# Performance work log

Hardware: AMD Instinct MI355X
Metric: run time of the kernel (lower is better)

The kernel has to match this reference:

```python
import jax, jax.numpy as jnp
import numpy as np

EMBEDDING_DIM = 512
MODEL_DIM = EMBEDDING_DIM
B, S = 32, 2048


def setup_inputs() -> dict:
    key = jax.random.key(0)
    ks = jax.random.split(key, 9)
    d, m = EMBEDDING_DIM, MODEL_DIM
    # xavier_uniform bounds
    def xavier(k, shape):
        fan_out, fan_in = shape
        lim = jnp.sqrt(6.0 / (fan_in + fan_out))
        return jax.random.uniform(k, shape, jnp.float32, -lim, lim)
    return {
        "query": jax.random.normal(ks[0], (B, d), jnp.float32),
        "keys": jax.random.normal(ks[1], (B, S, 2 * d), jnp.float32),
        "key_padding_mask": jax.random.randint(ks[2], (B, S), 0, 2) > 0,
        "Wa_w": xavier(ks[3], (m, d)),
        "Wa_b": jnp.zeros((m,), jnp.float32),
        "Ua_w": xavier(ks[4], (m, 2 * d)),
        "Ua_b": jnp.zeros((m,), jnp.float32),
        "Va_w": xavier(ks[5], (1, m)),
        "Va_b": jnp.zeros((1,), jnp.float32),
    }


def reference(query, keys, key_padding_mask, Wa_w, Wa_b, Ua_w, Ua_b, Va_w, Va_b):
    # Wa(query): [B, M]; Ua(keys): [B, S, M]
    wq = query @ Wa_w.T + Wa_b                      # [B, M]
    uk = jnp.einsum('bse,me->bsm', keys, Ua_w) + Ua_b  # [B, S, M]
    e = jnp.tanh(wq[:, None, :] + uk)               # [B, S, M]
    scores = jnp.einsum('bsm,om->bos', e, Va_w) + Va_b[None, :, None]  # [B, 1, S]
    scores = jnp.where(key_padding_mask[:, None, :], -jnp.inf, scores)
    attn = jax.nn.softmax(scores, axis=-1)          # [B, 1, S]
    context = jnp.einsum('bos,bse->boe', attn, keys)  # [B, 1, 2*EMBEDDING_DIM]
    return context
```

## Files before the change

### kernel.cpp

```cpp
#include <hip/hip_runtime.h>
#include <hip/hip_bf16.h>
#include <cstdint>
#include <cstddef>

#define B_   32
#define S_   2048
#define D_   512
#define K2D  1024
#define M_   512

#define WS_WQ     0
#define WS_FLAG   16384
#define WS_DENOM  16448
#define WS_UAB16  16512

typedef __attribute__((ext_vector_type(8))) short bf16x8;
typedef __attribute__((ext_vector_type(4))) float f32x4;

__device__ __forceinline__ float tanh_fast(float x) {
    float e = __expf(2.0f * x);
    return 1.0f - 2.0f * __builtin_amdgcn_rcpf(e + 1.0f);
}

union Pack8 { bf16x8 v; __hip_bfloat162 h[4]; };
__device__ __forceinline__ bf16x8 cvt8(float4 a, float4 b) {
    Pack8 p;
    p.h[0] = __float22bfloat162_rn(make_float2(a.x, a.y));
    p.h[1] = __float22bfloat162_rn(make_float2(a.z, a.w));
    p.h[2] = __float22bfloat162_rn(make_float2(b.x, b.y));
    p.h[3] = __float22bfloat162_rn(make_float2(b.z, b.w));
    return p.v;
}

__device__ __forceinline__ void gl_lds16(const void* g, void* l) {
    __builtin_amdgcn_global_load_lds(
        (const __attribute__((address_space(1))) unsigned int*)g,
        (__attribute__((address_space(3))) unsigned int*)l, 16, 0, 0);
}

__global__ __launch_bounds__(256) void k_prep(const float* __restrict__ query,
                                              const float* __restrict__ Wa_w,
                                              const float* __restrict__ Wa_b,
                                              const unsigned int* __restrict__ maskw,
                                              const float* __restrict__ Ua_w,
                                              float* __restrict__ wq,
                                              float* __restrict__ out,
                                              int* __restrict__ flag,
                                              float* __restrict__ denom,
                                              ushort* __restrict__ Ub16) {
    const int blk = blockIdx.x, t = threadIdx.x;
    if (blk < 256) {
        const int tid = blk * 256 + t;
        if (tid < 32768) out[tid] = 0.f;
        if (tid < 32) denom[tid] = 0.f;
        const int o = tid >> 2, sub = tid & 3;
        const int bq = o >> 9, m = o & 511;
        const float4* q = (const float4*)(query + (size_t)bq * D_ + sub * 128);
        const float4* w = (const float4*)(Wa_w + (size_t)m * D_ + sub * 128);
        float acc = 0.f;
#pragma unroll 8
        for (int i = 0; i < 32; ++i) {
            float4 qv = q[i], wv = w[i];
            acc = fmaf(qv.x, wv.x, acc);
            acc = fmaf(qv.y, wv.y, acc);
            acc = fmaf(qv.z, wv.z, acc);
            acc = fmaf(qv.w, wv.w, acc);
        }
        acc += __shfl_down(acc, 2, 64);
        acc += __shfl_down(acc, 1, 64);
        if (sub == 0) wq[o] = acc + Wa_b[m];
    } else if (blk == 256) {
        __shared__ int found;
        if (t == 0) found = 0;
        __syncthreads();
        int f = 0;
#pragma unroll
        for (int i = 0; i < 8; ++i)
            if (maskw[i * 256 + t] > 1u) f = 1;
        if (f) atomicOr(&found, 1);
        __syncthreads();
        if (t == 0) *flag = found;
    } else {
        const int i = ((blk - 257) * 256 + t) * 8;
        float4 a = *(const float4*)(Ua_w + i);
        float4 b = *(const float4*)(Ua_w + i + 4);
        *(bf16x8*)(Ub16 + i) = cvt8(a, b);
    }
}

__global__ __launch_bounds__(512, 2) void k_main(const float* __restrict__ keys,
                                                 const ushort* __restrict__ Ub16,
                                                 const float* __restrict__ Ua_b,
                                                 const float* __restrict__ Va_w,
                                                 const float* __restrict__ wq,
                                                 const void* __restrict__ mask,
                                                 const int* __restrict__ flag,
                                                 float* __restrict__ denom,
                                                 float* __restrict__ out) {
    __shared__ __align__(16) unsigned char smem[163840];
    unsigned char* Abase = smem;
    unsigned char* Bbase = smem + 32768;

    const int grp = blockIdx.x;
    const int b   = grp >> 4;
    const int s0  = (grp & 15) * 128;

    const int t = threadIdx.x;
    const int wave = t >> 6, lane = t & 63;
    const int q = lane >> 4, r = lane & 15;
    const int sw = (wave >> 2) * 64;
    const int mw = (wave & 3) * 128;

    const int arow = t >> 2, ac = (t & 3) * 2;
    const float* Ag = keys + ((size_t)(b * S_ + s0 + arow)) * K2D + ac * 8;
    const int ad0 = arow * 128 + ((ac ^ (arow & 7)) * 16);
    const int ad1 = arow * 128 + (((ac + 1) ^ (arow & 7)) * 16);

    const int brl = lane >> 3, bcl = lane & 7;
    const ushort* Bg = Ub16 + (size_t)(64 * wave + brl) * K2D + (bcl ^ brl) * 8;

    f32x4 acc[4][8];
#pragma unroll
    for (int i = 0; i < 4; ++i)
#pragma unroll
        for (int j = 0; j < 8; ++j) acc[i][j] = (f32x4){0.f, 0.f, 0.f, 0.f};

    {
        const float4* g = (const float4*)Ag;
        float4 f0 = g[0], f1 = g[1], f2 = g[2], f3 = g[3];
#pragma unroll
        for (int p = 0; p < 8; ++p)
            gl_lds16(Bg + (size_t)(8 * p) * K2D,
                     Bbase + (64 * wave + 8 * p) * 128);
        *(bf16x8*)(Abase + ad0) = cvt8(f0, f1);
        *(bf16x8*)(Abase + ad1) = cvt8(f2, f3);
        __syncthreads();
    }

    for (int kt = 0; kt < 16; ++kt) {
        const int cur = kt & 1, nxt = cur ^ 1;
        unsigned char* Acur = Abase + cur * 16384;
        unsigned char* Bcur = Bbase + cur * 65536;

        float4 f0, f1, f2, f3;
        if (kt < 15) {
            const int ko = (kt + 1) * 64;
            const float4* g = (const float4*)(Ag + ko);
            f0 = g[0]; f1 = g[1]; f2 = g[2]; f3 = g[3];
#pragma unroll
            for (int p = 0; p < 8; ++p)
                gl_lds16(Bg + (size_t)(8 * p) * K2D + ko,
                         Bbase + nxt * 65536 + (64 * wave + 8 * p) * 128);
        }

#pragma unroll
        for (int ks = 0; ks < 2; ++ks) {
            bf16x8 af[4], bf[8];
            const int lc = ks * 4 + q;
            const int pco = ((lc ^ (r & 7)) * 16);
#pragma unroll
            for (int i = 0; i < 4; ++i)
                af[i] = *(const bf16x8*)(Acur + (sw + i * 16 + r) * 128 + pco);
#pragma unroll
            for (int j = 0; j < 8; ++j)
                bf[j] = *(const bf16x8*)(Bcur + (mw + j * 16 + r) * 128 + pco);
#pragma unroll
            for (int i = 0; i < 4; ++i)
#pragma unroll
                for (int j = 0; j < 8; ++j)
                    acc[i][j] = __builtin_amdgcn_mfma_f32_16x16x32_bf16(
                        af[i], bf[j], acc[i][j], 0, 0, 0);
        }

        if (kt < 15) {
            unsigned char* An = Abase + nxt * 16384;
            *(bf16x8*)(An + ad0) = cvt8(f0, f1);
            *(bf16x8*)(An + ad1) = cvt8(f2, f3);
        }
        __syncthreads();
    }

    float vaw[8], wqb[8];
#pragma unroll
    for (int j = 0; j < 8; ++j) {
        int m = mw + 16 * j + r;
        vaw[j] = Va_w[m];
        wqb[j] = wq[b * M_ + m] + Ua_b[m];
    }
    float* red = (float*)smem;
    const int col = (wave & 3) * 16 + r;
#pragma unroll
    for (int i = 0; i < 4; ++i) {
#pragma unroll
        for (int rg = 0; rg < 4; ++rg) {
            int sl = sw + 16 * i + 4 * q + rg;
            float p = 0.f;
#pragma unroll
            for (int j = 0; j < 8; ++j)
                p += vaw[j] * tanh_fast(acc[i][j][rg] + wqb[j]);
            red[sl * 65 + col] = p;
        }
    }
    __syncthreads();

    float* wbuf = (float*)(smem + 33280);
    const bool bytemode = (*flag) != 0;
    if (t < 128) {
        float sum = 0.f;
#pragma unroll
        for (int c = 0; c < 64; ++c) sum += red[t * 65 + c];
        const size_t idx = (size_t)b * S_ + s0 + t;
        const bool msk = bytemode
            ? (((const unsigned char*)mask)[idx] != 0)
            : (((const int*)mask)[idx] != 0);
        wbuf[t] = msk ? 0.f : expf(sum);
    }
    __syncthreads();

    if (t < 64) {
        float s2 = wbuf[t] + wbuf[t + 64];
#pragma unroll
        for (int off = 32; off > 0; off >>= 1) s2 += __shfl_down(s2, off, 64);
        if (t == 0) atomicAdd(&denom[b], s2);
    }

    const float2* kp = (const float2*)(keys + ((size_t)b * S_ + s0) * K2D);
    float2 a2 = {0.f, 0.f};
#pragma unroll 8
    for (int s = 0; s < 128; ++s) {
        const float w2 = wbuf[s];
        const float2 kv = kp[(size_t)s * 512 + t];
        a2.x = fmaf(w2, kv.x, a2.x);
        a2.y = fmaf(w2, kv.y, a2.y);
    }
    atomicAdd(&out[b * 1024 + 2 * t + 0], a2.x);
    atomicAdd(&out[b * 1024 + 2 * t + 1], a2.y);
}

__global__ __launch_bounds__(256) void k_norm(float* __restrict__ out,
                                              const float* __restrict__ denom) {
    const int b = blockIdx.x, t = threadIdx.x;
    const float inv = 1.0f / denom[b];
    float4* o = (float4*)(out + (size_t)b * 1024);
    float4 v = o[t];
    v.x *= inv; v.y *= inv; v.z *= inv; v.w *= inv;
    o[t] = v;
}

extern "C" void kernel_launch(void* const* d_in, const int* in_sizes, int n_in,
                              void* d_out, int out_size, void* d_ws, size_t ws_size,
                              hipStream_t stream) {
    const float* query = (const float*)d_in[0];
    const float* keys  = (const float*)d_in[1];
    const void*  mask  = d_in[2];
    const float* Wa_w  = (const float*)d_in[3];
    const float* Wa_b  = (const float*)d_in[4];
    const float* Ua_w  = (const float*)d_in[5];
    const float* Ua_b  = (const float*)d_in[6];
    const float* Va_w  = (const float*)d_in[7];

    float*  wsf    = (float*)d_ws;
    float*  wq     = wsf + WS_WQ;
    int*    flag   = (int*)(wsf + WS_FLAG);
    float*  denom  = wsf + WS_DENOM;
    ushort* Ub16   = (ushort*)(wsf + WS_UAB16);
    float*  out    = (float*)d_out;

    k_prep<<<513, 256, 0, stream>>>(query, Wa_w, Wa_b,
                                    (const unsigned int*)mask, Ua_w,
                                    wq, out, flag, denom, Ub16);
    k_main<<<512, 512, 0, stream>>>(keys, Ub16, Ua_b, Va_w, wq,
                                    mask, flag, denom, out);
    k_norm<<<32, 256, 0, stream>>>(out, denom);
}
```

Measured before the change: 457.0 us.

## Interleave GEMM main loop into four MFMA phases with staggered LDS prefetch

The K-loop of the Ua GEMM is split into four phases, each loading a slice of B fragments from LDS and running its MFMAs. The async global-to-LDS copies for the next tile and the A-tile conversion are spread across the phases. Full __syncthreads barriers are replaced with explicit s_waitcnt vmcnt/lgkmcnt, raw s_barrier, sched_barrier and setprio, so memory traffic overlaps with matrix work. This risks subtle synchronization hazards: the vmcnt(4) count must match the outstanding loads, and the wave writing the next A tile must not race other waves still reading.

```diff
diff --git a/kernel.cpp b/kernel.cpp
--- a/kernel.cpp
+++ b/kernel.cpp
@@ -134,51 +134,144 @@
                      Bbase + (64 * wave + 8 * p) * 128);
         *(bf16x8*)(Abase + ad0) = cvt8(f0, f1);
         *(bf16x8*)(Abase + ad1) = cvt8(f2, f3);
-        __syncthreads();
+        asm volatile("s_waitcnt lgkmcnt(0)" ::: "memory");
     }
 
     for (int kt = 0; kt < 16; ++kt) {
         const int cur = kt & 1, nxt = cur ^ 1;
         unsigned char* Acur = Abase + cur * 16384;
         unsigned char* Bcur = Bbase + cur * 65536;
+        unsigned char* Bnxt = Bbase + nxt * 65536;
+        const int ko = (kt + 1) * 64;
 
         float4 f0, f1, f2, f3;
         if (kt < 15) {
-            const int ko = (kt + 1) * 64;
             const float4* g = (const float4*)(Ag + ko);
             f0 = g[0]; f1 = g[1]; f2 = g[2]; f3 = g[3];
-#pragma unroll
-            for (int p = 0; p < 8; ++p)
-                gl_lds16(Bg + (size_t)(8 * p) * K2D + ko,
-                         Bbase + nxt * 65536 + (64 * wave + 8 * p) * 128);
-        }
-
-#pragma unroll
-        for (int ks = 0; ks < 2; ++ks) {
-            bf16x8 af[4], bf[8];
-            const int lc = ks * 4 + q;
-            const int pco = ((lc ^ (r & 7)) * 16);
-#pragma unroll
-            for (int i = 0; i < 4; ++i)
-                af[i] = *(const bf16x8*)(Acur + (sw + i * 16 + r) * 128 + pco);
-#pragma unroll
-            for (int j = 0; j < 8; ++j)
-                bf[j] = *(const bf16x8*)(Bcur + (mw + j * 16 + r) * 128 + pco);
-#pragma unroll
-            for (int i = 0; i < 4; ++i)
-#pragma unroll
-                for (int j = 0; j < 8; ++j)
-                    acc[i][j] = __builtin_amdgcn_mfma_f32_16x16x32_bf16(
-                        af[i], bf[j], acc[i][j], 0, 0, 0);
-        }
-
-        if (kt < 15) {
-            unsigned char* An = Abase + nxt * 16384;
-            *(bf16x8*)(An + ad0) = cvt8(f0, f1);
-            *(bf16x8*)(An + ad1) = cvt8(f2, f3);
-        }
-        __syncthreads();
-    }
+            asm volatile("s_waitcnt vmcnt(4)" ::: "memory");
+        } else {
+            asm volatile("s_waitcnt vmcnt(0)" ::: "memory");
+        }
+        __builtin_amdgcn_s_barrier();
+        __builtin_amdgcn_sched_barrier(0);
+
+        bf16x8 af[2][4];
+        {
+            bf16x8 bfp[2][2];
+#pragma unroll
+            for (int ks = 0; ks < 2; ++ks) {
+                const int pco = (((ks * 4 + q) ^ (r & 7)) * 16);
+#pragma unroll
+                for (int i = 0; i < 4; ++i)
+                    af[ks][i] = *(const bf16x8*)(Acur + (sw + i * 16 + r) * 128 + pco);
+#pragma unroll
+                for (int jj = 0; jj < 2; ++jj)
+                    bfp[ks][jj] = *(const bf16x8*)(Bcur + (mw + jj * 16 + r) * 128 + pco);
+            }
+            if (kt < 15) {
+#pragma unroll
+                for (int p = 0; p < 4; ++p)
+                    gl_lds16(Bg + (size_t)(8 * p) * K2D + ko,
+                             Bnxt + (64 * wave + 8 * p) * 128);
+            }
+            asm volatile("s_waitcnt lgkmcnt(0)" ::: "memory");
+            __builtin_amdgcn_sched_barrier(0);
+            __builtin_amdgcn_s_setprio(1);
+#pragma unroll
+            for (int ks = 0; ks < 2; ++ks)
+#pragma unroll
+                for (int i = 0; i < 4; ++i)
+#pragma unroll
+                    for (int jj = 0; jj < 2; ++jj)
+                        acc[i][jj] = __builtin_amdgcn_mfma_f32_16x16x32_bf16(
+                            af[ks][i], bfp[ks][jj], acc[i][jj], 0, 0, 0);
+            __builtin_amdgcn_s_setprio(0);
+        }
+        __builtin_amdgcn_s_barrier();
+        __builtin_amdgcn_sched_barrier(0);
+        {
+            bf16x8 bfp[2][2];
+#pragma unroll
+            for (int ks = 0; ks < 2; ++ks) {
+                const int pco = (((ks * 4 + q) ^ (r & 7)) * 16);
+#pragma unroll
+                for (int jj = 0; jj < 2; ++jj)
+                    bfp[ks][jj] = *(const bf16x8*)(Bcur + (mw + (2 + jj) * 16 + r) * 128 + pco);
+            }
+            if (kt < 15) {
+#pragma unroll
+                for (int p = 4; p < 8; ++p)
+                    gl_lds16(Bg + (size_t)(8 * p) * K2D + ko,
+                             Bnxt + (64 * wave + 8 * p) * 128);
+            }
+            asm volatile("s_waitcnt lgkmcnt(0)" ::: "memory");
+            __builtin_amdgcn_sched_barrier(0);
+            __builtin_amdgcn_s_setprio(1);
+#pragma unroll
+            for (int ks = 0; ks < 2; ++ks)
+#pragma unroll
+                for (int i = 0; i < 4; ++i)
+#pragma unroll
+                    for (int jj = 0; jj < 2; ++jj)
+                        acc[i][2 + jj] = __builtin_amdgcn_mfma_f32_16x16x32_bf16(
+                            af[ks][i], bfp[ks][jj], acc[i][2 + jj], 0, 0, 0);
+            __builtin_amdgcn_s_setprio(0);
+        }
+        __builtin_amdgcn_s_barrier();
+        __builtin_amdgcn_sched_barrier(0);
+        {
+            bf16x8 bfp[2][2];
+#pragma unroll
+            for (int ks = 0; ks < 2; ++ks) {
+                const int pco = (((ks * 4 + q) ^ (r & 7)) * 16);
+#pragma unroll
+                for (int jj = 0; jj < 2; ++jj)
+                    bfp[ks][jj] = *(const bf16x8*)(Bcur + (mw + (4 + jj) * 16 + r) * 128 + pco);
+            }
+            if (kt < 15) {
+                unsigned char* An = Abase + nxt * 16384;
+                *(bf16x8*)(An + ad0) = cvt8(f0, f1);
+                *(bf16x8*)(An + ad1) = cvt8(f2, f3);
+            }
+            asm volatile("s_waitcnt lgkmcnt(0)" ::: "memory");
+            __builtin_amdgcn_sched_barrier(0);
+            __builtin_amdgcn_s_setprio(1);
+#pragma unroll
+            for (int ks = 0; ks < 2; ++ks)
+#pragma unroll
+                for (int i = 0; i < 4; ++i)
+#pragma unroll
+                    for (int jj = 0; jj < 2; ++jj)
+                        acc[i][4 + jj] = __builtin_amdgcn_mfma_f32_16x16x32_bf16(
+                            af[ks][i], bfp[ks][jj], acc[i][4 + jj], 0, 0, 0);
+            __builtin_amdgcn_s_setprio(0);
+        }
+        __builtin_amdgcn_s_barrier();
+        __builtin_amdgcn_sched_barrier(0);
+        {
+            bf16x8 bfp[2][2];
+#pragma unroll
+            for (int ks = 0; ks < 2; ++ks) {
+                const int pco = (((ks * 4 + q) ^ (r & 7)) * 16);
+#pragma unroll
+                for (int jj = 0; jj < 2; ++jj)
+                    bfp[ks][jj] = *(const bf16x8*)(Bcur + (mw + (6 + jj) * 16 + r) * 128 + pco);
+            }
+            asm volatile("s_waitcnt lgkmcnt(0)" ::: "memory");
+            __builtin_amdgcn_sched_barrier(0);
+            __builtin_amdgcn_s_setprio(1);
+#pragma unroll
+            for (int ks = 0; ks < 2; ++ks)
+#pragma unroll
+                for (int i = 0; i < 4; ++i)
+#pragma unroll
+                    for (int jj = 0; jj < 2; ++jj)
+                        acc[i][6 + jj] = __builtin_amdgcn_mfma_f32_16x16x32_bf16(
+                            af[ks][i], bfp[ks][jj], acc[i][6 + jj], 0, 0, 0);
+            __builtin_amdgcn_s_setprio(0);
+        }
+    }
+    __syncthreads();
 
     float vaw[8], wqb[8];
 #pragma unroll
```

Result: slower. 476.7 us (+4.3%).

## Halve main-kernel S tile and K step to fit more blocks per CU

Applied to the files above, without the earlier changes.

Reworks the fused score/context kernel so each block handles 64 sequence rows instead of 128, with a K step of 32 instead of 64. LDS per block shrinks from 160KB to 80KB, the grid doubles to 1024 blocks and launch bounds ask for more resident blocks. Each wave now computes a 64x64 tile over all 64 rows, with a new swizzled LDS layout. The aim is better occupancy and latency hiding, at the cost of less B-operand reuse per block (Ua weights are reloaded twice as often), more sync steps and twice as many output atomics.

```diff
diff --git a/kernel.cpp b/kernel.cpp
--- a/kernel.cpp
+++ b/kernel.cpp
@@ -15,6 +15,7 @@
 #define WS_UAB16  16512
 
 typedef __attribute__((ext_vector_type(8))) short bf16x8;
+typedef __attribute__((ext_vector_type(4))) short bf16x4;
 typedef __attribute__((ext_vector_type(4))) float f32x4;
 
 __device__ __forceinline__ float tanh_fast(float x) {
@@ -29,6 +30,13 @@
     p.h[1] = __float22bfloat162_rn(make_float2(a.z, a.w));
     p.h[2] = __float22bfloat162_rn(make_float2(b.x, b.y));
     p.h[3] = __float22bfloat162_rn(make_float2(b.z, b.w));
+    return p.v;
+}
+union Pack4 { bf16x4 v; __hip_bfloat162 h[2]; };
+__device__ __forceinline__ bf16x4 cvt4(float4 a) {
+    Pack4 p;
+    p.h[0] = __float22bfloat162_rn(make_float2(a.x, a.y));
+    p.h[1] = __float22bfloat162_rn(make_float2(a.z, a.w));
     return p.v;
 }
 
@@ -88,7 +96,7 @@
     }
 }
 
-__global__ __launch_bounds__(512, 2) void k_main(const float* __restrict__ keys,
+__global__ __launch_bounds__(512, 4) void k_main(const float* __restrict__ keys,
                                                  const ushort* __restrict__ Ub16,
                                                  const float* __restrict__ Ua_b,
                                                  const float* __restrict__ Va_w,
@@ -97,137 +105,138 @@
                                                  const int* __restrict__ flag,
                                                  float* __restrict__ denom,
                                                  float* __restrict__ out) {
-    __shared__ __align__(16) unsigned char smem[163840];
+    __shared__ __align__(16) unsigned char smem[81920];
     unsigned char* Abase = smem;
-    unsigned char* Bbase = smem + 32768;
+    unsigned char* Bbase = smem + 8192;
 
     const int grp = blockIdx.x;
-    const int b   = grp >> 4;
-    const int s0  = (grp & 15) * 128;
+    const int b   = grp >> 5;
+    const int s0  = (grp & 31) * 64;
 
     const int t = threadIdx.x;
     const int wave = t >> 6, lane = t & 63;
     const int q = lane >> 4, r = lane & 15;
-    const int sw = (wave >> 2) * 64;
-    const int mw = (wave & 3) * 128;
-
-    const int arow = t >> 2, ac = (t & 3) * 2;
-    const float* Ag = keys + ((size_t)(b * S_ + s0 + arow)) * K2D + ac * 8;
-    const int ad0 = arow * 128 + ((ac ^ (arow & 7)) * 16);
-    const int ad1 = arow * 128 + (((ac + 1) ^ (arow & 7)) * 16);
+    const int mw = wave * 64;
+
+    const int as   = t >> 3, akq = t & 7;
+    const float* Ag = keys + ((size_t)(b * S_ + s0 + as)) * K2D + akq * 4;
+    const int arho = as & 31;
+    const int ast  = arho * 128 +
+                     (((4 * (as >> 5) + (akq >> 1)) ^ (arho & 7)) * 16) +
+                     (akq & 1) * 8;
 
     const int brl = lane >> 3, bcl = lane & 7;
-    const ushort* Bg = Ub16 + (size_t)(64 * wave + brl) * K2D + (bcl ^ brl) * 8;
-
-    f32x4 acc[4][8];
+    const int bclog = bcl ^ (brl & 7);
+    const int bm0 = 32 * wave + brl + 256 * (bclog >> 2);
+    const ushort* Bg = Ub16 + (size_t)bm0 * K2D + (bclog & 3) * 8;
+    const int bdst = (32 * wave) * 128 + lane * 16;
+
+    int aoff[4], boff[4];
+#pragma unroll
+    for (int i = 0; i < 4; ++i) {
+        const int s = 16 * i + r, rho = s & 31;
+        aoff[i] = rho * 128 + (((4 * (s >> 5) + q) ^ (rho & 7)) * 16);
+    }
+#pragma unroll
+    for (int j = 0; j < 4; ++j) {
+        const int m = mw + 16 * j + r, rho = m & 255;
+        boff[j] = rho * 128 + (((4 * (m >> 8) + q) ^ (rho & 7)) * 16);
+    }
+
+    f32x4 acc[4][4];
 #pragma unroll
     for (int i = 0; i < 4; ++i)
 #pragma unroll
-        for (int j = 0; j < 8; ++j) acc[i][j] = (f32x4){0.f, 0.f, 0.f, 0.f};
+        for (int j = 0; j < 4; ++j) acc[i][j] = (f32x4){0.f, 0.f, 0.f, 0.f};
 
     {
-        const float4* g = (const float4*)Ag;
-        float4 f0 = g[0], f1 = g[1], f2 = g[2], f3 = g[3];
-#pragma unroll
-        for (int p = 0; p < 8; ++p)
-            gl_lds16(Bg + (size_t)(8 * p) * K2D,
-                     Bbase + (64 * wave + 8 * p) * 128);
-        *(bf16x8*)(Abase + ad0) = cvt8(f0, f1);
-        *(bf16x8*)(Abase + ad1) = cvt8(f2, f3);
-        __syncthreads();
-    }
-
-    for (int kt = 0; kt < 16; ++kt) {
+        float4 av = *(const float4*)Ag;
+#pragma unroll
+        for (int p = 0; p < 4; ++p)
+            gl_lds16(Bg + (size_t)p * 8 * K2D, Bbase + bdst + p * 1024);
+        *(bf16x4*)(Abase + ast) = cvt4(av);
+        __syncthreads();
+    }
+
+    for (int kt = 0; kt < 32; ++kt) {
         const int cur = kt & 1, nxt = cur ^ 1;
-        unsigned char* Acur = Abase + cur * 16384;
-        unsigned char* Bcur = Bbase + cur * 65536;
-
-        float4 f0, f1, f2, f3;
-        if (kt < 15) {
-            const int ko = (kt + 1) * 64;
-            const float4* g = (const float4*)(Ag + ko);
-            f0 = g[0]; f1 = g[1]; f2 = g[2]; f3 = g[3];
-#pragma unroll
-            for (int p = 0; p < 8; ++p)
-                gl_lds16(Bg + (size_t)(8 * p) * K2D + ko,
-                         Bbase + nxt * 65536 + (64 * wave + 8 * p) * 128);
+        unsigned char* Acur = Abase + cur * 4096;
+        unsigned char* Bcur = Bbase + cur * 32768;
+
+        float4 av;
+        if (kt < 31) {
+            const int ko = (kt + 1) * 32;
+            av = *(const float4*)(Ag + ko);
+#pragma unroll
+            for (int p = 0; p < 4; ++p)
+                gl_lds16(Bg + (size_t)p * 8 * K2D + ko,
+                         Bbase + nxt * 32768 + bdst + p * 1024);
         }
 
-#pragma unroll
-        for (int ks = 0; ks < 2; ++ks) {
-            bf16x8 af[4], bf[8];
-            const int lc = ks * 4 + q;
-            const int pco = ((lc ^ (r & 7)) * 16);
-#pragma unroll
-            for (int i = 0; i < 4; ++i)
-                af[i] = *(const bf16x8*)(Acur + (sw + i * 16 + r) * 128 + pco);
-#pragma unroll
-            for (int j = 0; j < 8; ++j)
-                bf[j] = *(const bf16x8*)(Bcur + (mw + j * 16 + r) * 128 + pco);
-#pragma unroll
-            for (int i = 0; i < 4; ++i)
-#pragma unroll
-                for (int j = 0; j < 8; ++j)
-                    acc[i][j] = __builtin_amdgcn_mfma_f32_16x16x32_bf16(
-                        af[i], bf[j], acc[i][j], 0, 0, 0);
-        }
-
-        if (kt < 15) {
-            unsigned char* An = Abase + nxt * 16384;
-            *(bf16x8*)(An + ad0) = cvt8(f0, f1);
-            *(bf16x8*)(An + ad1) = cvt8(f2, f3);
-        }
-        __syncthreads();
-    }
-
-    float vaw[8], wqb[8];
-#pragma unroll
-    for (int j = 0; j < 8; ++j) {
+        bf16x8 af[4], bf[4];
+#pragma unroll
+        for (int i = 0; i < 4; ++i)
+            af[i] = *(const bf16x8*)(Acur + aoff[i]);
+#pragma unroll
+        for (int j = 0; j < 4; ++j)
+            bf[j] = *(const bf16x8*)(Bcur + boff[j]);
+#pragma unroll
+        for (int i = 0; i < 4; ++i)
+#pragma unroll
+            for (int j = 0; j < 4; ++j)
+                acc[i][j] = __builtin_amdgcn_mfma_f32_16x16x32_bf16(
+                    af[i], bf[j], acc[i][j], 0, 0, 0);
+
+        if (kt < 31)
+            *(bf16x4*)(Abase + nxt * 4096 + ast) = cvt4(av);
+        __syncthreads();
+    }
+
+    float vaw[4], wqb[4];
+#pragma unroll
+    for (int j = 0; j < 4; ++j) {
         int m = mw + 16 * j + r;
         vaw[j] = Va_w[m];
         wqb[j] = wq[b * M_ + m] + Ua_b[m];
     }
     float* red = (float*)smem;
-    const int col = (wave & 3) * 16 + r;
+    const int col = wave * 16 + r;
 #pragma unroll
     for (int i = 0; i < 4; ++i) {
 #pragma unroll
         for (int rg = 0; rg < 4; ++rg) {
-            int sl = sw + 16 * i + 4 * q + rg;
+            int sl = 16 * i + 4 * q + rg;
             float p = 0.f;
 #pragma unroll
-            for (int j = 0; j < 8; ++j)
+            for (int j = 0; j < 4; ++j)
                 p += vaw[j] * tanh_fast(acc[i][j][rg] + wqb[j]);
-            red[sl * 65 + col] = p;
+            red[sl * 129 + col] = p;
         }
     }
     __syncthreads();
 
-    float* wbuf = (float*)(smem + 33280);
+    float* wbuf = (float*)(smem + 33024);
     const bool bytemode = (*flag) != 0;
-    if (t < 128) {
+    if (t < 64) {
         float sum = 0.f;
 #pragma unroll
-        for (int c = 0; c < 64; ++c) sum += red[t * 65 + c];
+        for (int c = 0; c < 128; ++c) sum += red[t * 129 + c];
         const size_t idx = (size_t)b * S_ + s0 + t;
         const bool msk = bytemode
             ? (((const unsigned char*)mask)[idx] != 0)
             : (((const int*)mask)[idx] != 0);
-        wbuf[t] = msk ? 0.f : expf(sum);
+        float v = msk ? 0.f : expf(sum);
+        wbuf[t] = v;
+#pragma unroll
+        for (int off = 32; off > 0; off >>= 1) v += __shfl_down(v, off, 64);
+        if (t == 0) atomicAdd(&denom[b], v);
     }
     __syncthreads();
-
-    if (t < 64) {
-        float s2 = wbuf[t] + wbuf[t + 64];
-#pragma unroll
-        for (int off = 32; off > 0; off >>= 1) s2 += __shfl_down(s2, off, 64);
-        if (t == 0) atomicAdd(&denom[b], s2);
-    }
 
     const float2* kp = (const float2*)(keys + ((size_t)b * S_ + s0) * K2D);
     float2 a2 = {0.f, 0.f};
 #pragma unroll 8
-    for (int s = 0; s < 128; ++s) {
+    for (int s = 0; s < 64; ++s) {
         const float w2 = wbuf[s];
         const float2 kv = kp[(size_t)s * 512 + t];
         a2.x = fmaf(w2, kv.x, a2.x);
@@ -269,7 +278,7 @@
     k_prep<<<513, 256, 0, stream>>>(query, Wa_w, Wa_b,
                                     (const unsigned int*)mask, Ua_w,
                                     wq, out, flag, denom, Ub16);
-    k_main<<<512, 512, 0, stream>>>(keys, Ub16, Ua_b, Va_w, wq,
-                                    mask, flag, denom, out);
+    k_main<<<1024, 512, 0, stream>>>(keys, Ub16, Ua_b, Va_w, wq,
+                                     mask, flag, denom, out);
     k_norm<<<32, 256, 0, stream>>>(out, denom);
 }
```

Result: slower. 475.9 us (+4.1%).
